# Optimization experiments

Hardware: AMD Instinct MI355X
Metric: run time of the kernel (lower is better)

The kernel has to match this reference:

```python
import math
import jax, jax.numpy as jnp
import numpy as np

ALPH = 0.8

def setup_inputs() -> dict:
    key = jax.random.key(0)
    k1, k2 = jax.random.split(key)
    B, C, N, T = 64, 64, 500, 48
    x = jax.random.normal(k1, (B, C, N, T), dtype=jnp.float32)
    s = jax.random.uniform(k2, (N, N), dtype=jnp.float32)
    return {"x": x, "s": s}

def reference(x, s):
    # x: [B, C, N, T], s: [N, N]
    B, C, N, T = x.shape
    # Row sums of the (never materialized) [N*T, N*T] supra-laplacian:
    # block row i, node v -> s.sum(axis=1)[v] + (T-1-i)*alph
    s_rowsum = s.sum(axis=1)                              # [N]
    time_term = (T - 1 - jnp.arange(T, dtype=jnp.float32)) * ALPH  # [T]
    rowsum = (time_term[:, None] + s_rowsum[None, :]).reshape(-1)  # [T*N], k = i*N+v
    # Faithful to original: x flattened as [B, C, N*T] (k = n*T + t), multiplied
    # elementwise by rowsum[k] (the 'bcn,nm->bcn' einsum reduces to this).
    x_window = x.reshape(B, C, N * T)
    x_window = jax.nn.relu(x_window * rowsum / math.sqrt(C))
    adj_dyn = jax.nn.softmax(x_window, axis=-1)            # [B, C, N*T]
    x_w_s = adj_dyn.reshape(B, C, N, T).sum(-1)            # [B, C, N]
    gram = jnp.einsum('bcn,bcm->bnm', x_w_s, x_w_s)        # [B, N, N]
    A_l = jax.nn.softmax(jax.nn.relu(gram) / math.sqrt(C), axis=-1)
    return A_l
```

## Files before the change

### kernel.cpp

```cpp
#include <hip/hip_runtime.h>
#include <math.h>

#define NN 500
#define TT 48
#define NT 24000
#define NF4 6000

__global__ void k_srow(const float* __restrict__ s, float* __restrict__ srow) {
    int r = blockIdx.x;
    int l = threadIdx.x;
    float v = 0.f;
    for (int j = l; j < NN; j += 64) v += s[r * NN + j];
    #pragma unroll
    for (int o = 32; o; o >>= 1) v += __shfl_xor(v, o);
    if (l == 0) srow[r] = v;
}

__launch_bounds__(512, 4)
__global__ void k_p1(const float* __restrict__ x, const float* __restrict__ srow,
                     float* __restrict__ xws) {
    __shared__ float p[6144];
    __shared__ __align__(16) float sr[512];
    __shared__ float redm[8], reds[8];
    int bc = blockIdx.x;
    int tid = threadIdx.x;
    int w = tid >> 6, l = tid & 63;
    int f0 = w * 768 + l;

    if (tid < NN) sr[tid] = srow[tid];
    __syncthreads();

    const float4* xp = (const float4*)x + (size_t)bc * NF4;

    float sf[12], ml[12];
    float m = 0.f;

    #pragma unroll
    for (int i = 0; i < 9; i++) {
        int f = f0 + i * 64;
        int kk = 4 * f;
        int ti = kk / 500;
        int v  = kk - ti * 500;
        float tt = (float)(TT - 1 - ti) * 0.8f;
        float4 sv = *(const float4*)(sr + v);
        float4 xv = xp[f];
        float y0 = fmaxf(xv.x * (tt + sv.x) * 0.125f, 0.f);
        float y1 = fmaxf(xv.y * (tt + sv.y) * 0.125f, 0.f);
        float y2 = fmaxf(xv.z * (tt + sv.z) * 0.125f, 0.f);
        float y3 = fmaxf(xv.w * (tt + sv.w) * 0.125f, 0.f);
        float mm = fmaxf(fmaxf(y0, y1), fmaxf(y2, y3));
        sf[i] = __expf(y0 - mm) + __expf(y1 - mm)
              + __expf(y2 - mm) + __expf(y3 - mm);
        ml[i] = mm;
        m = fmaxf(m, mm);
    }
    #pragma unroll
    for (int i = 9; i < 12; i++) {
        int f = f0 + i * 64;
        int fc = (f < NF4) ? f : (NF4 - 1);
        float msk = (f < NF4) ? 1.f : 0.f;
        int kk = 4 * fc;
        int ti = kk / 500;
        int v  = kk - ti * 500;
        float tt = (float)(TT - 1 - ti) * 0.8f;
        float4 sv = *(const float4*)(sr + v);
        float4 xv = xp[fc];
        float y0 = fmaxf(xv.x * (tt + sv.x) * 0.125f, 0.f);
        float y1 = fmaxf(xv.y * (tt + sv.y) * 0.125f, 0.f);
        float y2 = fmaxf(xv.z * (tt + sv.z) * 0.125f, 0.f);
        float y3 = fmaxf(xv.w * (tt + sv.w) * 0.125f, 0.f);
        float mm = fmaxf(fmaxf(y0, y1), fmaxf(y2, y3));
        float sfi = __expf(y0 - mm) + __expf(y1 - mm)
                  + __expf(y2 - mm) + __expf(y3 - mm);
        sf[i] = sfi * msk;
        ml[i] = mm;
        m = fmaxf(m, mm);
    }

    #pragma unroll
    for (int o = 32; o; o >>= 1) m = fmaxf(m, __shfl_xor(m, o));
    if (l == 0) redm[w] = m;
    __syncthreads();
    float M = redm[0];
    #pragma unroll
    for (int i = 1; i < 8; i++) M = fmaxf(M, redm[i]);

    float tot = 0.f;
    #pragma unroll
    for (int i = 0; i < 12; i++) {
        float cf = sf[i] * __expf(ml[i] - M);
        p[f0 + i * 64] = cf;
        tot += cf;
    }
    #pragma unroll
    for (int o = 32; o; o >>= 1) tot += __shfl_xor(tot, o);
    if (l == 0) reds[w] = tot;
    __syncthreads();
    float Z = 0.f;
    #pragma unroll
    for (int i = 0; i < 8; i++) Z += reds[i];

    if (tid < NN) {
        const float* pp = p + tid * 12;
        float sn = 0.f;
        #pragma unroll
        for (int j = 0; j < 12; j++) sn += pp[j];
        xws[(size_t)bc * NN + tid] = sn / Z;
    }
}

__launch_bounds__(512, 4)
__global__ void k_p2(const float* __restrict__ xws, float* __restrict__ out) {
    __shared__ __align__(16) float Xs[32 * NN + 16];
    int b = blockIdx.y;
    int rt8 = blockIdx.x;
    int tid = threadIdx.x;

    int rt = tid >> 6, cx = tid & 63;
    int r0 = rt8 * 64 + rt * 8;
    int cb0 = cx * 4, cb1 = cx * 4 + 256;

    float acc[8][8];
    #pragma unroll
    for (int i = 0; i < 8; i++)
        #pragma unroll
        for (int j = 0; j < 8; j++) acc[i][j] = 0.f;

    for (int cbk = 0; cbk < 2; cbk++) {
        const float4* src4 = (const float4*)(xws + ((size_t)b * 64 + 32 * cbk) * NN);
        __syncthreads();
        #pragma unroll
        for (int i = 0; i < 8; i++) {
            int idx = tid + i * 512;
            if (idx < 4000) ((float4*)Xs)[idx] = src4[idx];
        }
        if (tid < 16) Xs[32 * NN + tid] = 0.f;
        __syncthreads();

        #pragma unroll 4
        for (int c = 0; c < 32; c++) {
            const float* row = Xs + c * NN;
            float4 a0 = *(const float4*)(row + r0);
            float4 a1 = *(const float4*)(row + r0 + 4);
            float4 b0 = *(const float4*)(row + cb0);
            float4 b1 = *(const float4*)(row + cb1);
            float av[8] = {a0.x, a0.y, a0.z, a0.w, a1.x, a1.y, a1.z, a1.w};
            float bv[8] = {b0.x, b0.y, b0.z, b0.w, b1.x, b1.y, b1.z, b1.w};
            #pragma unroll
            for (int i = 0; i < 8; i++)
                #pragma unroll
                for (int j = 0; j < 8; j++)
                    acc[i][j] = fmaf(av[i], bv[j], acc[i][j]);
        }
    }

    bool c1v = (cx <= 60);
    size_t ob = (size_t)b * (NN * NN);
    #pragma unroll 1
    for (int ri = 0; ri < 8; ri++) {
        int r = r0 + ri;
        if (r >= NN) break;
        float u[8];
        #pragma unroll
        for (int j = 0; j < 8; j++) u[j] = fmaxf(acc[ri][j], 0.f) * 0.125f;
        float mx = fmaxf(fmaxf(u[0], u[1]), fmaxf(u[2], u[3]));
        if (c1v) mx = fmaxf(mx, fmaxf(fmaxf(u[4], u[5]), fmaxf(u[6], u[7])));
        #pragma unroll
        for (int o = 32; o; o >>= 1) mx = fmaxf(mx, __shfl_xor(mx, o));

        float e[8];
        float es = 0.f;
        #pragma unroll
        for (int j = 0; j < 4; j++) { e[j] = __expf(u[j] - mx); es += e[j]; }
        if (c1v) {
            #pragma unroll
            for (int j = 4; j < 8; j++) { e[j] = __expf(u[j] - mx); es += e[j]; }
        }
        #pragma unroll
        for (int o = 32; o; o >>= 1) es += __shfl_xor(es, o);
        float inv = 1.f / es;

        float4 w0 = make_float4(e[0] * inv, e[1] * inv, e[2] * inv, e[3] * inv);
        *(float4*)(out + ob + (size_t)r * NN + cb0) = w0;
        if (c1v) {
            float4 w1 = make_float4(e[4] * inv, e[5] * inv, e[6] * inv, e[7] * inv);
            *(float4*)(out + ob + (size_t)r * NN + cb1) = w1;
        }
    }
}

extern "C" void kernel_launch(void* const* d_in, const int* in_sizes, int n_in,
                              void* d_out, int out_size, void* d_ws, size_t ws_size,
                              hipStream_t stream) {
    const float* x = (const float*)d_in[0];
    const float* s = (const float*)d_in[1];
    float* out = (float*)d_out;
    float* wsf = (float*)d_ws;

    float* srow = wsf;
    float* xws  = wsf + 32768;

    k_srow<<<NN, 64, 0, stream>>>(s, srow);
    k_p1<<<64 * 64, 512, 0, stream>>>(x, srow, xws);
    dim3 g2(8, 64);
    k_p2<<<g2, 512, 0, stream>>>(xws, out);
}
```

Before: 166.8 us.

## Process two (b,c) rows per 256-thread block in softmax-sum kernel

The first-pass kernel now uses 256-thread blocks, each handling two consecutive (b,c) rows in a loop with 24 float4 loads per thread, and launches half as many blocks. The final per-node reduction reads shared memory as float4 and multiplies by a precomputed reciprocal of Z. The Gram/softmax kernel's launch bound drops from 4 to 2 blocks per CU, allowing more registers. The intent is to cut block scheduling and setup overhead and raise memory-level parallelism per thread, at the cost of higher register pressure and fewer resident threads.

New measurement: 286.1 us. 71.5% more time.

```diff
diff --git a/kernel.cpp b/kernel.cpp
--- a/kernel.cpp
+++ b/kernel.cpp
@@ -5,6 +5,8 @@
 #define TT 48
 #define NT 24000
 #define NF4 6000
+
+typedef float f4v __attribute__((ext_vector_type(4)));
 
 __global__ void k_srow(const float* __restrict__ s, float* __restrict__ srow) {
     int r = blockIdx.x;
@@ -16,100 +18,87 @@
     if (l == 0) srow[r] = v;
 }
 
-__launch_bounds__(512, 4)
+__launch_bounds__(256, 4)
 __global__ void k_p1(const float* __restrict__ x, const float* __restrict__ srow,
                      float* __restrict__ xws) {
-    __shared__ float p[6144];
+    __shared__ __align__(16) float p[6144];
     __shared__ __align__(16) float sr[512];
-    __shared__ float redm[8], reds[8];
-    int bc = blockIdx.x;
+    __shared__ float red[8];
+    int g = blockIdx.x;
     int tid = threadIdx.x;
     int w = tid >> 6, l = tid & 63;
-    int f0 = w * 768 + l;
 
-    if (tid < NN) sr[tid] = srow[tid];
+    sr[tid] = srow[(tid < NN) ? tid : (NN - 1)];
+    int t2 = tid + 256;
+    sr[t2] = (t2 < NN) ? srow[t2] : 0.f;
     __syncthreads();
 
-    const float4* xp = (const float4*)x + (size_t)bc * NF4;
+    #pragma unroll 1
+    for (int rr = 0; rr < 2; ++rr) {
+        int bc = g * 2 + rr;
+        const f4v* xp = (const f4v*)x + (size_t)bc * NF4;
 
-    float sf[12], ml[12];
-    float m = 0.f;
+        float sf[24], ml[24];
+        float m = 0.f;
+        #pragma unroll
+        for (int i = 0; i < 24; i++) {
+            int f = i * 256 + tid;
+            int fc = (f < NF4) ? f : (NF4 - 1);
+            float msk = (f < NF4) ? 1.f : 0.f;
+            f4v xv = xp[fc];
+            int kk = 4 * fc;
+            int ti = kk / 500;
+            int v  = kk - ti * 500;
+            float tt = (float)(TT - 1 - ti) * 0.8f;
+            float4 sv = *(const float4*)(sr + v);
+            float y0 = fmaxf(xv.x * (tt + sv.x) * 0.125f, 0.f);
+            float y1 = fmaxf(xv.y * (tt + sv.y) * 0.125f, 0.f);
+            float y2 = fmaxf(xv.z * (tt + sv.z) * 0.125f, 0.f);
+            float y3 = fmaxf(xv.w * (tt + sv.w) * 0.125f, 0.f);
+            float mm = fmaxf(fmaxf(y0, y1), fmaxf(y2, y3));
+            float sfi = __expf(y0 - mm) + __expf(y1 - mm)
+                      + __expf(y2 - mm) + __expf(y3 - mm);
+            sf[i] = sfi * msk;
+            ml[i] = mm;
+            m = fmaxf(m, mm);
+        }
 
-    #pragma unroll
-    for (int i = 0; i < 9; i++) {
-        int f = f0 + i * 64;
-        int kk = 4 * f;
-        int ti = kk / 500;
-        int v  = kk - ti * 500;
-        float tt = (float)(TT - 1 - ti) * 0.8f;
-        float4 sv = *(const float4*)(sr + v);
-        float4 xv = xp[f];
-        float y0 = fmaxf(xv.x * (tt + sv.x) * 0.125f, 0.f);
-        float y1 = fmaxf(xv.y * (tt + sv.y) * 0.125f, 0.f);
-        float y2 = fmaxf(xv.z * (tt + sv.z) * 0.125f, 0.f);
-        float y3 = fmaxf(xv.w * (tt + sv.w) * 0.125f, 0.f);
-        float mm = fmaxf(fmaxf(y0, y1), fmaxf(y2, y3));
-        sf[i] = __expf(y0 - mm) + __expf(y1 - mm)
-              + __expf(y2 - mm) + __expf(y3 - mm);
-        ml[i] = mm;
-        m = fmaxf(m, mm);
-    }
-    #pragma unroll
-    for (int i = 9; i < 12; i++) {
-        int f = f0 + i * 64;
-        int fc = (f < NF4) ? f : (NF4 - 1);
-        float msk = (f < NF4) ? 1.f : 0.f;
-        int kk = 4 * fc;
-        int ti = kk / 500;
-        int v  = kk - ti * 500;
-        float tt = (float)(TT - 1 - ti) * 0.8f;
-        float4 sv = *(const float4*)(sr + v);
-        float4 xv = xp[fc];
-        float y0 = fmaxf(xv.x * (tt + sv.x) * 0.125f, 0.f);
-        float y1 = fmaxf(xv.y * (tt + sv.y) * 0.125f, 0.f);
-        float y2 = fmaxf(xv.z * (tt + sv.z) * 0.125f, 0.f);
-        float y3 = fmaxf(xv.w * (tt + sv.w) * 0.125f, 0.f);
-        float mm = fmaxf(fmaxf(y0, y1), fmaxf(y2, y3));
-        float sfi = __expf(y0 - mm) + __expf(y1 - mm)
-                  + __expf(y2 - mm) + __expf(y3 - mm);
-        sf[i] = sfi * msk;
-        ml[i] = mm;
-        m = fmaxf(m, mm);
-    }
+        #pragma unroll
+        for (int o = 32; o; o >>= 1) m = fmaxf(m, __shfl_xor(m, o));
+        if (l == 0) red[w] = m;
+        __syncthreads();
+        float M = fmaxf(fmaxf(red[0], red[1]), fmaxf(red[2], red[3]));
 
-    #pragma unroll
-    for (int o = 32; o; o >>= 1) m = fmaxf(m, __shfl_xor(m, o));
-    if (l == 0) redm[w] = m;
-    __syncthreads();
-    float M = redm[0];
-    #pragma unroll
-    for (int i = 1; i < 8; i++) M = fmaxf(M, redm[i]);
+        float tot = 0.f;
+        #pragma unroll
+        for (int i = 0; i < 24; i++) {
+            float cf = sf[i] * __expf(ml[i] - M);
+            p[i * 256 + tid] = cf;
+            tot += cf;
+        }
+        #pragma unroll
+        for (int o = 32; o; o >>= 1) tot += __shfl_xor(tot, o);
+        if (l == 0) red[4 + w] = tot;
+        __syncthreads();
+        float Z = (red[4] + red[5]) + (red[6] + red[7]);
+        float invZ = 1.f / Z;
 
-    float tot = 0.f;
-    #pragma unroll
-    for (int i = 0; i < 12; i++) {
-        float cf = sf[i] * __expf(ml[i] - M);
-        p[f0 + i * 64] = cf;
-        tot += cf;
-    }
-    #pragma unroll
-    for (int o = 32; o; o >>= 1) tot += __shfl_xor(tot, o);
-    if (l == 0) reds[w] = tot;
-    __syncthreads();
-    float Z = 0.f;
-    #pragma unroll
-    for (int i = 0; i < 8; i++) Z += reds[i];
-
-    if (tid < NN) {
-        const float* pp = p + tid * 12;
-        float sn = 0.f;
         #pragma unroll
-        for (int j = 0; j < 12; j++) sn += pp[j];
-        xws[(size_t)bc * NN + tid] = sn / Z;
+        for (int q = 0; q < 2; ++q) {
+            int n = tid + q * 256;
+            if (n < NN) {
+                const float4* pp = (const float4*)(p + n * 12);
+                float4 a = pp[0], b4 = pp[1], c4 = pp[2];
+                float sn = a.x + a.y + a.z + a.w + b4.x + b4.y + b4.z + b4.w
+                         + c4.x + c4.y + c4.z + c4.w;
+                xws[(size_t)bc * NN + n] = sn * invZ;
+            }
+        }
+        __syncthreads();
     }
 }
 
-__launch_bounds__(512, 4)
+__launch_bounds__(512, 2)
 __global__ void k_p2(const float* __restrict__ xws, float* __restrict__ out) {
     __shared__ __align__(16) float Xs[32 * NN + 16];
     int b = blockIdx.y;
@@ -201,7 +190,7 @@
     float* xws  = wsf + 32768;
 
     k_srow<<<NN, 64, 0, stream>>>(s, srow);
-    k_p1<<<64 * 64, 512, 0, stream>>>(x, srow, xws);
+    k_p1<<<2048, 256, 0, stream>>>(x, srow, xws);
     dim3 g2(8, 64);
     k_p2<<<g2, 512, 0, stream>>>(xws, out);
 }
```
